# Kernel tuning notes

Measured on AMD Instinct MI355X. Metric: run time of the kernel, lower is better.

Reference implementation:

```python
import jax, jax.numpy as jnp
import numpy as np


def setup_inputs() -> dict:
    key = jax.random.key(0)
    k1, k2 = jax.random.split(key)
    x = jax.random.normal(k1, (16, 512, 64, 64), dtype=jnp.float32)
    gamma = jax.random.normal(k2, (1,), dtype=jnp.float32) * 0.05  # 'random_normal' init
    return {"x": x, "gamma": gamma}


def reference(x, gamma):
    # x: (B, C, H, W); code path is channels_last, C taken from x.shape[1]
    B, C, H, W = x.shape
    N = H * W
    # Reshape((-1, C)) is a flat row-major reshape -> (B, N, C)
    q = x.reshape(B, N, C)  # query == key == value (same tensor)
    # energy = matmul(query, key, transpose_a=True) -> (B, C, C)
    energy = jnp.einsum('bnc,bnd->bcd', q, q)
    # reduce_max(energy, axis=1, keepdims=True)[0]: max over axis 1 then take
    # FIRST BATCH element -> shape (1, C), broadcast against (B, C, C)
    mx = jnp.max(energy, axis=1, keepdims=True)[0]  # (1, C)
    energy_2 = mx - energy  # (B, C, C)
    # Keras Activation('softmax') -> softmax over last axis
    attention = jax.nn.softmax(energy_2, axis=-1)  # (B, C, C)
    # matmul(attention, value, transpose_b=True): (B,C,C) @ (B,C,N) -> (B,C,N)
    out = jnp.einsum('bcd,bnd->bcn', attention, q)
    # Reshape back to x.shape[1:] = (C, H, W) (flat reshape, N = H*W)
    out = out.reshape(B, C, H, W)
    return gamma * out + x
```

## Files before the change

kernel.cpp:

```cpp
#include <hip/hip_runtime.h>
#include <cstdint>

#define B_DIM 16
#define C_DIM 512
#define N_DIM 4096

typedef __bf16 bf16x8 __attribute__((ext_vector_type(8)));
typedef unsigned short u16x8 __attribute__((ext_vector_type(8)));
typedef unsigned short u16x4 __attribute__((ext_vector_type(4)));
typedef unsigned int u32x4 __attribute__((ext_vector_type(4)));
typedef unsigned int u32x2 __attribute__((ext_vector_type(2)));
typedef float f32x4 __attribute__((ext_vector_type(4)));

__device__ __forceinline__ bf16x8 as_bf(u16x8 v) { return __builtin_bit_cast(bf16x8, v); }

__device__ __forceinline__ unsigned pack_hi(unsigned ua, unsigned ub) {
    return __builtin_amdgcn_perm(ub, ua, 0x07060302u);
}
__device__ __forceinline__ unsigned rne_pack(float a, float b) {
    unsigned ua = __float_as_uint(a);
    ua += 0x7fffu + ((ua >> 16) & 1u);
    unsigned ub = __float_as_uint(b);
    ub += 0x7fffu + ((ub >> 16) & 1u);
    return pack_hi(ua, ub);
}

#define BT 128
#define BK 32
#define BKP 40

__global__ __launch_bounds__(256) void gram_kernel(const float* __restrict__ x,
                                                   float* __restrict__ part, int kshift) {
    const int nwg = 10 * gridDim.z;
    const int chunk = nwg >> 3;
    const int flat = blockIdx.x + 10 * blockIdx.z;
    const int swz = (flat & 7) * chunk + (flat >> 3);
    const int tile = swz % 10;
    const int z = swz / 10;
    const int s = z & ((1 << kshift) - 1);
    const int b = z >> kshift;
    static const int TI[10] = {0, 0, 0, 0, 1, 1, 1, 2, 2, 3};
    static const int TJ[10] = {0, 1, 2, 3, 1, 2, 3, 2, 3, 3};
    const int c0 = TI[tile] * BT;
    const int d0 = TJ[tile] * BT;
    const bool diag = (c0 == d0);

    const float* __restrict__ Q = x + (size_t)b * (N_DIM * C_DIM);
    float* __restrict__ E = part + ((size_t)s * B_DIM + b) * (C_DIM * C_DIM);

    __shared__ unsigned short lAh[BT][BKP];
    __shared__ unsigned short lAl[BT][BKP];
    __shared__ unsigned short lBh[BT][BKP];
    __shared__ unsigned short lBl[BT][BKP];

    const int tid = threadIdx.x;
    const int lane = tid & 63;
    const int w = tid >> 6;
    const int moff = (w & 1) * 64;
    const int noff = (w >> 1) * 64;
    const int frow = lane & 15;
    const int fk = (lane >> 4) * 8;

    f32x4 acc[4][4];
#pragma unroll
    for (int m = 0; m < 4; ++m)
#pragma unroll
        for (int n = 0; n < 4; ++n) acc[m][n] = (f32x4){0.f, 0.f, 0.f, 0.f};

    const int cc = tid & 127;
    const int kh = tid >> 7;

    const int klen = N_DIM >> kshift;
    const float* gA = Q + (size_t)(s * klen + kh * 16) * C_DIM + (c0 + cc);
    const float* gB = Q + (size_t)(s * klen + kh * 16) * C_DIM + (d0 + cc);

    const unsigned short(*pBh)[BKP] = diag ? lAh : lBh;
    const unsigned short(*pBl)[BKP] = diag ? lAl : lBl;

    float av[16], bv[16];
#pragma unroll
    for (int i = 0; i < 16; ++i) av[i] = gA[(size_t)i * C_DIM];
    if (!diag) {
#pragma unroll
        for (int i = 0; i < 16; ++i) bv[i] = gB[(size_t)i * C_DIM];
    }
    gA += (size_t)BK * C_DIM;
    gB += (size_t)BK * C_DIM;

    const int T = klen / BK;
    for (int t = 0; t < T; ++t) {
        u32x4 ah[2], al[2], bh[2], bl[2];
#pragma unroll
        for (int g = 0; g < 2; ++g)
#pragma unroll
            for (int p = 0; p < 4; ++p) {
                const int j = g * 8 + p * 2;
                unsigned u0 = __float_as_uint(av[j]), u1 = __float_as_uint(av[j + 1]);
                ah[g][p] = pack_hi(u0, u1);
                float r0 = av[j] - __uint_as_float(u0 & 0xffff0000u);
                float r1 = av[j + 1] - __uint_as_float(u1 & 0xffff0000u);
                al[g][p] = pack_hi(__float_as_uint(r0), __float_as_uint(r1));
            }
        if (!diag) {
#pragma unroll
            for (int g = 0; g < 2; ++g)
#pragma unroll
                for (int p = 0; p < 4; ++p) {
                    const int j = g * 8 + p * 2;
                    unsigned u0 = __float_as_uint(bv[j]), u1 = __float_as_uint(bv[j + 1]);
                    bh[g][p] = pack_hi(u0, u1);
                    float r0 = bv[j] - __uint_as_float(u0 & 0xffff0000u);
                    float r1 = bv[j + 1] - __uint_as_float(u1 & 0xffff0000u);
                    bl[g][p] = pack_hi(__float_as_uint(r0), __float_as_uint(r1));
                }
        }

        __syncthreads();
        *(u16x8*)&lAh[cc][kh * 16]     = __builtin_bit_cast(u16x8, ah[0]);
        *(u16x8*)&lAh[cc][kh * 16 + 8] = __builtin_bit_cast(u16x8, ah[1]);
        *(u16x8*)&lAl[cc][kh * 16]     = __builtin_bit_cast(u16x8, al[0]);
        *(u16x8*)&lAl[cc][kh * 16 + 8] = __builtin_bit_cast(u16x8, al[1]);
        if (!diag) {
            *(u16x8*)&lBh[cc][kh * 16]     = __builtin_bit_cast(u16x8, bh[0]);
            *(u16x8*)&lBh[cc][kh * 16 + 8] = __builtin_bit_cast(u16x8, bh[1]);
            *(u16x8*)&lBl[cc][kh * 16]     = __builtin_bit_cast(u16x8, bl[0]);
            *(u16x8*)&lBl[cc][kh * 16 + 8] = __builtin_bit_cast(u16x8, bl[1]);
        }
        __syncthreads();

        if (t + 1 < T) {
#pragma unroll
            for (int i = 0; i < 16; ++i) av[i] = gA[(size_t)i * C_DIM];
            if (!diag) {
#pragma unroll
                for (int i = 0; i < 16; ++i) bv[i] = gB[(size_t)i * C_DIM];
            }
            gA += (size_t)BK * C_DIM;
            gB += (size_t)BK * C_DIM;
        }

        bf16x8 fbh[4], fbl[4];
#pragma unroll
        for (int n = 0; n < 4; ++n) {
            fbh[n] = as_bf(*(const u16x8*)&pBh[noff + n * 16 + frow][fk]);
            fbl[n] = as_bf(*(const u16x8*)&pBl[noff + n * 16 + frow][fk]);
        }
#pragma unroll
        for (int m = 0; m < 4; ++m) {
            bf16x8 fah = as_bf(*(const u16x8*)&lAh[moff + m * 16 + frow][fk]);
            bf16x8 fal = as_bf(*(const u16x8*)&lAl[moff + m * 16 + frow][fk]);
#pragma unroll
            for (int n = 0; n < 4; ++n) {
                acc[m][n] = __builtin_amdgcn_mfma_f32_16x16x32_bf16(fah, fbh[n], acc[m][n], 0, 0, 0);
                acc[m][n] = __builtin_amdgcn_mfma_f32_16x16x32_bf16(fah, fbl[n], acc[m][n], 0, 0, 0);
                acc[m][n] = __builtin_amdgcn_mfma_f32_16x16x32_bf16(fal, fbh[n], acc[m][n], 0, 0, 0);
            }
        }
    }

#pragma unroll
    for (int m = 0; m < 4; ++m)
#pragma unroll
        for (int n = 0; n < 4; ++n) {
            const int r = c0 + moff + m * 16 + (lane >> 4) * 4;
            const int col = d0 + noff + n * 16 + frow;
#pragma unroll
            for (int i = 0; i < 4; ++i)
                E[(size_t)(r + i) * C_DIM + col] = acc[m][n][i];
        }
    if (!diag) {
#pragma unroll
        for (int m = 0; m < 4; ++m)
#pragma unroll
            for (int n = 0; n < 4; ++n) {
                const int r = c0 + moff + m * 16 + (lane >> 4) * 4;
                const int col = d0 + noff + n * 16 + frow;
#pragma unroll
                for (int i = 0; i < 4; ++i)
                    E[(size_t)col * C_DIM + (r + i)] = acc[m][n][i];
            }
    }
}

__global__ __launch_bounds__(256) void colmax1(const float* __restrict__ part,
                                               float* __restrict__ pmax, int sk) {
    const int d = blockIdx.x * 256 + threadIdx.x;
    const int cg = blockIdx.y;
    const size_t PS = (size_t)B_DIM * C_DIM * C_DIM;
    float m = -3.4e38f;
    for (int c = cg * 64; c < cg * 64 + 64; ++c) {
        float e = 0.f;
        for (int s = 0; s < sk; ++s) e += part[(size_t)s * PS + (size_t)c * C_DIM + d];
        m = fmaxf(m, e);
    }
    pmax[cg * C_DIM + d] = m;
}

__global__ __launch_bounds__(256) void colmax2(const float* __restrict__ pmax,
                                               float* __restrict__ mx) {
    const int d = blockIdx.x * 256 + threadIdx.x;
    float m = pmax[d];
#pragma unroll
    for (int g = 1; g < 8; ++g) m = fmaxf(m, pmax[g * C_DIM + d]);
    mx[d] = m;
}

__global__ __launch_bounds__(256) void softmax_kernel(float* __restrict__ part,
                                                      const float* __restrict__ mx, int sk) {
    const int wid = blockIdx.x * 4 + (threadIdx.x >> 6);
    const int lane = threadIdx.x & 63;
    const size_t PS = (size_t)B_DIM * C_DIM * C_DIM;

    f32x4 ea = (f32x4){0.f, 0.f, 0.f, 0.f}, eb = ea;
    for (int s = 0; s < sk; ++s) {
        const f32x4* row = (const f32x4*)(part + (size_t)s * PS + (size_t)wid * C_DIM + lane * 8);
        ea += row[0];
        eb += row[1];
    }
    f32x4 ma = *(const f32x4*)&mx[lane * 8];
    f32x4 mb = *(const f32x4*)&mx[lane * 8 + 4];

    float v[8];
#pragma unroll
    for (int j = 0; j < 4; ++j) v[j] = ma[j] - ea[j];
#pragma unroll
    for (int j = 0; j < 4; ++j) v[4 + j] = mb[j] - eb[j];

    float rm = v[0];
#pragma unroll
    for (int j = 1; j < 8; ++j) rm = fmaxf(rm, v[j]);
#pragma unroll
    for (int st = 1; st < 64; st <<= 1) rm = fmaxf(rm, __shfl_xor(rm, st));

    float p[8];
    float sum = 0.f;
#pragma unroll
    for (int j = 0; j < 8; ++j) {
        p[j] = expf(v[j] - rm);
        sum += p[j];
    }
#pragma unroll
    for (int st = 1; st < 64; st <<= 1) sum += __shfl_xor(sum, st);

    const float inv = 1.f / sum;
    u32x4 o;
#pragma unroll
    for (int q = 0; q < 4; ++q) o[q] = rne_pack(p[2 * q] * inv, p[2 * q + 1] * inv);
    unsigned short* arow = (unsigned short*)part + (size_t)wid * 1024 + 512;
    *(u16x8*)&arow[lane * 8] = __builtin_bit_cast(u16x8, o);
}

__global__ __launch_bounds__(256, 4) void gemm2_kernel(const unsigned short* __restrict__ att16,
                                                       const float* __restrict__ x,
                                                       const float* __restrict__ gamma,
                                                       float* __restrict__ out) {
    const int flat = blockIdx.x + 4 * (blockIdx.y + 32 * blockIdx.z);
    const int swz = (flat & 7) * 256 + (flat >> 3);
    const int c0 = (swz & 3) * BT;
    const int n0 = ((swz >> 2) & 31) * BT;
    const int b = swz >> 7;

    const float* __restrict__ Q = x + (size_t)b * (N_DIM * C_DIM);
    const float* __restrict__ Xb = Q;
    float* __restrict__ Ob = out + (size_t)b * (C_DIM * N_DIM);
    const unsigned short* __restrict__ Ab = att16 + (size_t)(b * C_DIM + c0) * 1024 + 512;

    __shared__ unsigned short lA[2][BT][BKP];
    __shared__ unsigned short lB[2][BT][BKP];

    const int tid = threadIdx.x;
    const int lane = tid & 63;
    const int w = tid >> 6;
    const int moff = (w & 1) * 64;
    const int noff = (w >> 1) * 64;
    const int frow = lane & 15;
    const int fk = (lane >> 4) * 8;

    f32x4 acc[4][4];
#pragma unroll
    for (int m = 0; m < 4; ++m)
#pragma unroll
        for (int n = 0; n < 4; ++n) acc[m][n] = (f32x4){0.f, 0.f, 0.f, 0.f};

    u16x8 pa[2];
    float4 rb[4];
#pragma unroll
    for (int i = 0; i < 2; ++i) {
        const int f = tid + 256 * i;
        pa[i] = *(const u16x8*)&Ab[(size_t)(f >> 2) * 1024 + ((f & 3) * 8)];
    }
#pragma unroll
    for (int i = 0; i < 4; ++i) {
        const int f = tid + 256 * i;
        rb[i] = *(const float4*)&Q[(size_t)(n0 + (f >> 3)) * C_DIM + ((f & 7) * 4)];
    }
#pragma unroll
    for (int i = 0; i < 2; ++i) {
        const int f = tid + 256 * i;
        *(u16x8*)&lA[0][f >> 2][(f & 3) * 8] = pa[i];
    }
#pragma unroll
    for (int i = 0; i < 4; ++i) {
        const int f = tid + 256 * i;
        u32x2 pk = {pack_hi(__float_as_uint(rb[i].x), __float_as_uint(rb[i].y)),
                    pack_hi(__float_as_uint(rb[i].z), __float_as_uint(rb[i].w))};
        *(u16x4*)&lB[0][f >> 3][(f & 7) * 4] = __builtin_bit_cast(u16x4, pk);
    }

    int cur = 0;
    for (int t = 0; t < 16; ++t) {
        __syncthreads();
        if (t < 15) {
            const int k1 = (t + 1) * BK;
#pragma unroll
            for (int i = 0; i < 2; ++i) {
                const int f = tid + 256 * i;
                pa[i] = *(const u16x8*)&Ab[(size_t)(f >> 2) * 1024 + k1 + ((f & 3) * 8)];
            }
#pragma unroll
            for (int i = 0; i < 4; ++i) {
                const int f = tid + 256 * i;
                rb[i] = *(const float4*)&Q[(size_t)(n0 + (f >> 3)) * C_DIM + k1 + ((f & 7) * 4)];
            }
        }

        bf16x8 fb[4];
#pragma unroll
        for (int n = 0; n < 4; ++n)
            fb[n] = as_bf(*(const u16x8*)&lB[cur][noff + n * 16 + frow][fk]);
#pragma unroll
        for (int m = 0; m < 4; ++m) {
            bf16x8 fa = as_bf(*(const u16x8*)&lA[cur][moff + m * 16 + frow][fk]);
#pragma unroll
            for (int n = 0; n < 4; ++n)
                acc[m][n] = __builtin_amdgcn_mfma_f32_16x16x32_bf16(fa, fb[n], acc[m][n], 0, 0, 0);
        }

        if (t < 15) {
            const int nb = cur ^ 1;
#pragma unroll
            for (int i = 0; i < 2; ++i) {
                const int f = tid + 256 * i;
                *(u16x8*)&lA[nb][f >> 2][(f & 3) * 8] = pa[i];
            }
#pragma unroll
            for (int i = 0; i < 4; ++i) {
                const int f = tid + 256 * i;
                u32x2 pk = {pack_hi(__float_as_uint(rb[i].x), __float_as_uint(rb[i].y)),
                            pack_hi(__float_as_uint(rb[i].z), __float_as_uint(rb[i].w))};
                *(u16x4*)&lB[nb][f >> 3][(f & 7) * 4] = __builtin_bit_cast(u16x4, pk);
            }
        }
        cur ^= 1;
    }

    const float g = gamma[0];
#pragma unroll
    for (int m = 0; m < 4; ++m)
#pragma unroll
        for (int n = 0; n < 4; ++n) {
            const int r = c0 + moff + m * 16 + (lane >> 4) * 4;
            const int col = n0 + noff + n * 16 + frow;
#pragma unroll
            for (int i = 0; i < 4; ++i) {
                const size_t idx = (size_t)(r + i) * N_DIM + col;
                Ob[idx] = g * acc[m][n][i] + Xb[idx];
            }
        }
}

extern "C" void kernel_launch(void* const* d_in, const int* in_sizes, int n_in,
                              void* d_out, int out_size, void* d_ws, size_t ws_size,
                              hipStream_t stream) {
    const float* x = (const float*)d_in[0];
    const float* gamma = (const float*)d_in[1];
    float* out = (float*)d_out;

    const size_t HDR = 32 * 1024;
    const size_t PSZ = (size_t)B_DIM * C_DIM * C_DIM * sizeof(float);
    int kshift = 0;
    if (ws_size >= HDR + 4 * PSZ) kshift = 2;
    else if (ws_size >= HDR + 2 * PSZ) kshift = 1;
    const int SK = 1 << kshift;

    float* mx = (float*)d_ws;
    float* pmax = mx + C_DIM;
    float* part = (float*)((char*)d_ws + HDR);

    dim3 g1(10, 1, B_DIM * SK);
    gram_kernel<<<g1, 256, 0, stream>>>(x, part, kshift);

    colmax1<<<dim3(2, 8), 256, 0, stream>>>(part, pmax, SK);
    colmax2<<<2, 256, 0, stream>>>(pmax, mx);

    softmax_kernel<<<(B_DIM * C_DIM) / 4, 256, 0, stream>>>(part, mx, SK);

    dim3 g2(C_DIM / BT, N_DIM / BT, B_DIM);
    gemm2_kernel<<<g2, 256, 0, stream>>>((const unsigned short*)part, x, gamma, out);
}
```

Before: 294.7 us.

## Stream gemm2 B tiles via global_load_lds and read A fragments directly

The second GEMM now copies fp32 x tiles straight into LDS with global_load_lds and an XOR swizzle, then converts them to bf16 when fragments are read, instead of staging through registers. Attention fragments are loaded from global memory into registers per lane, which removes the A LDS buffer and its stores. The launch becomes a 1D grid, the occupancy hint is dropped, and the barrier moves to the end of each iteration. This cuts register staging and LDS write traffic, but adds conversion work on every fragment read and puts uncoalesced global loads for A on the critical path.

```diff
diff --git a/kernel.cpp b/kernel.cpp
--- a/kernel.cpp
+++ b/kernel.cpp
@@ -23,6 +23,11 @@
     unsigned ub = __float_as_uint(b);
     ub += 0x7fffu + ((ub >> 16) & 1u);
     return pack_hi(ua, ub);
+}
+
+__device__ __forceinline__ void gload_lds16(const void* g, void* l) {
+    __builtin_amdgcn_global_load_lds((const __attribute__((address_space(1))) void*)g,
+                                     (__attribute__((address_space(3))) void*)l, 16, 0, 0);
 }
 
 #define BT 128
@@ -250,23 +255,21 @@
     *(u16x8*)&arow[lane * 8] = __builtin_bit_cast(u16x8, o);
 }
 
-__global__ __launch_bounds__(256, 4) void gemm2_kernel(const unsigned short* __restrict__ att16,
-                                                       const float* __restrict__ x,
-                                                       const float* __restrict__ gamma,
-                                                       float* __restrict__ out) {
-    const int flat = blockIdx.x + 4 * (blockIdx.y + 32 * blockIdx.z);
+__global__ __launch_bounds__(256) void gemm2_kernel(const unsigned short* __restrict__ att16,
+                                                    const float* __restrict__ x,
+                                                    const float* __restrict__ gamma,
+                                                    float* __restrict__ out) {
+    const int flat = blockIdx.x;
     const int swz = (flat & 7) * 256 + (flat >> 3);
     const int c0 = (swz & 3) * BT;
     const int n0 = ((swz >> 2) & 31) * BT;
     const int b = swz >> 7;
 
     const float* __restrict__ Q = x + (size_t)b * (N_DIM * C_DIM);
-    const float* __restrict__ Xb = Q;
     float* __restrict__ Ob = out + (size_t)b * (C_DIM * N_DIM);
     const unsigned short* __restrict__ Ab = att16 + (size_t)(b * C_DIM + c0) * 1024 + 512;
 
-    __shared__ unsigned short lA[2][BT][BKP];
-    __shared__ unsigned short lB[2][BT][BKP];
+    __shared__ float lB[2][BT][BK];
 
     const int tid = threadIdx.x;
     const int lane = tid & 63;
@@ -274,7 +277,11 @@
     const int moff = (w & 1) * 64;
     const int noff = (w >> 1) * 64;
     const int frow = lane & 15;
-    const int fk = (lane >> 4) * 8;
+    const int fq = lane >> 4;
+
+    const int srow = (w << 3) + (lane >> 3);
+    const int scol = (((lane & 7) ^ (lane >> 3)) << 2);
+    const int sdst = w * 256 + lane * 4;
 
     f32x4 acc[4][4];
 #pragma unroll
@@ -282,75 +289,57 @@
 #pragma unroll
         for (int n = 0; n < 4; ++n) acc[m][n] = (f32x4){0.f, 0.f, 0.f, 0.f};
 
-    u16x8 pa[2];
-    float4 rb[4];
-#pragma unroll
-    for (int i = 0; i < 2; ++i) {
-        const int f = tid + 256 * i;
-        pa[i] = *(const u16x8*)&Ab[(size_t)(f >> 2) * 1024 + ((f & 3) * 8)];
-    }
-#pragma unroll
-    for (int i = 0; i < 4; ++i) {
-        const int f = tid + 256 * i;
-        rb[i] = *(const float4*)&Q[(size_t)(n0 + (f >> 3)) * C_DIM + ((f & 7) * 4)];
-    }
-#pragma unroll
-    for (int i = 0; i < 2; ++i) {
-        const int f = tid + 256 * i;
-        *(u16x8*)&lA[0][f >> 2][(f & 3) * 8] = pa[i];
-    }
-#pragma unroll
-    for (int i = 0; i < 4; ++i) {
-        const int f = tid + 256 * i;
-        u32x2 pk = {pack_hi(__float_as_uint(rb[i].x), __float_as_uint(rb[i].y)),
-                    pack_hi(__float_as_uint(rb[i].z), __float_as_uint(rb[i].w))};
-        *(u16x4*)&lB[0][f >> 3][(f & 7) * 4] = __builtin_bit_cast(u16x4, pk);
-    }
+    const unsigned short* Arow[4];
+#pragma unroll
+    for (int m = 0; m < 4; ++m)
+        Arow[m] = Ab + (size_t)(moff + m * 16 + frow) * 1024 + fq * 8;
+
+#pragma unroll
+    for (int i = 0; i < 4; ++i)
+        gload_lds16(&Q[(size_t)(n0 + srow + 32 * i) * C_DIM + scol],
+                    (float*)&lB[0][0][0] + sdst + 1024 * i);
+    u16x8 paC[4], paN[4];
+#pragma unroll
+    for (int m = 0; m < 4; ++m) paC[m] = *(const u16x8*)(Arow[m]);
+    __syncthreads();
 
     int cur = 0;
     for (int t = 0; t < 16; ++t) {
-        __syncthreads();
         if (t < 15) {
             const int k1 = (t + 1) * BK;
 #pragma unroll
-            for (int i = 0; i < 2; ++i) {
-                const int f = tid + 256 * i;
-                pa[i] = *(const u16x8*)&Ab[(size_t)(f >> 2) * 1024 + k1 + ((f & 3) * 8)];
-            }
-#pragma unroll
-            for (int i = 0; i < 4; ++i) {
-                const int f = tid + 256 * i;
-                rb[i] = *(const float4*)&Q[(size_t)(n0 + (f >> 3)) * C_DIM + k1 + ((f & 7) * 4)];
-            }
+            for (int i = 0; i < 4; ++i)
+                gload_lds16(&Q[(size_t)(n0 + srow + 32 * i) * C_DIM + k1 + scol],
+                            (float*)&lB[cur ^ 1][0][0] + sdst + 1024 * i);
+#pragma unroll
+            for (int m = 0; m < 4; ++m) paN[m] = *(const u16x8*)(Arow[m] + k1);
         }
 
         bf16x8 fb[4];
 #pragma unroll
-        for (int n = 0; n < 4; ++n)
-            fb[n] = as_bf(*(const u16x8*)&lB[cur][noff + n * 16 + frow][fk]);
+        for (int n = 0; n < 4; ++n) {
+            const int rr = noff + n * 16 + frow;
+            const int sx = rr & 7;
+            const float4 b0 = *(const float4*)&lB[cur][rr][((2 * fq) ^ sx) << 2];
+            const float4 b1 = *(const float4*)&lB[cur][rr][((2 * fq + 1) ^ sx) << 2];
+            u32x4 pk = {pack_hi(__float_as_uint(b0.x), __float_as_uint(b0.y)),
+                        pack_hi(__float_as_uint(b0.z), __float_as_uint(b0.w)),
+                        pack_hi(__float_as_uint(b1.x), __float_as_uint(b1.y)),
+                        pack_hi(__float_as_uint(b1.z), __float_as_uint(b1.w))};
+            fb[n] = as_bf(__builtin_bit_cast(u16x8, pk));
+        }
 #pragma unroll
         for (int m = 0; m < 4; ++m) {
-            bf16x8 fa = as_bf(*(const u16x8*)&lA[cur][moff + m * 16 + frow][fk]);
+            const bf16x8 fa = as_bf(paC[m]);
 #pragma unroll
             for (int n = 0; n < 4; ++n)
                 acc[m][n] = __builtin_amdgcn_mfma_f32_16x16x32_bf16(fa, fb[n], acc[m][n], 0, 0, 0);
         }
-
         if (t < 15) {
-            const int nb = cur ^ 1;
-#pragma unroll
-            for (int i = 0; i < 2; ++i) {
-                const int f = tid + 256 * i;
-                *(u16x8*)&lA[nb][f >> 2][(f & 3) * 8] = pa[i];
-            }
-#pragma unroll
-            for (int i = 0; i < 4; ++i) {
-                const int f = tid + 256 * i;
-                u32x2 pk = {pack_hi(__float_as_uint(rb[i].x), __float_as_uint(rb[i].y)),
-                            pack_hi(__float_as_uint(rb[i].z), __float_as_uint(rb[i].w))};
-                *(u16x4*)&lB[nb][f >> 3][(f & 7) * 4] = __builtin_bit_cast(u16x4, pk);
-            }
-        }
+#pragma unroll
+            for (int m = 0; m < 4; ++m) paC[m] = paN[m];
+        }
+        __syncthreads();
         cur ^= 1;
     }
 
@@ -359,12 +348,12 @@
     for (int m = 0; m < 4; ++m)
 #pragma unroll
         for (int n = 0; n < 4; ++n) {
-            const int r = c0 + moff + m * 16 + (lane >> 4) * 4;
+            const int r = c0 + moff + m * 16 + fq * 4;
             const int col = n0 + noff + n * 16 + frow;
 #pragma unroll
             for (int i = 0; i < 4; ++i) {
                 const size_t idx = (size_t)(r + i) * N_DIM + col;
-                Ob[idx] = g * acc[m][n][i] + Xb[idx];
+                Ob[idx] = g * acc[m][n][i] + Q[idx];
             }
         }
 }
@@ -395,6 +384,5 @@
 
     softmax_kernel<<<(B_DIM * C_DIM) / 4, 256, 0, stream>>>(part, mx, SK);
 
-    dim3 g2(C_DIM / BT, N_DIM / BT, B_DIM);
-    gemm2_kernel<<<g2, 256, 0, stream>>>((const unsigned short*)part, x, gamma, out);
-}
+    gemm2_kernel<<<2048, 256, 0, stream>>>((const unsigned short*)part, x, gamma, out);
+}
```

Result: slower. 316.2 us (+7.3%).
